# Performance work log

Measured on AMD Instinct MI355X. Metric: run time of the kernel, lower is better.

The kernel has to match this reference:

```python
import jax, jax.numpy as jnp
import numpy as np

N = 50000
E = 400000  # bidirectional: second half is reverse of first half
D = 128
T = 3
EPS = 1e-09


def apply_lambda(x, log_dt, log_lambda_real, lambda_imag, one_minus=False):
    # lambda_complex = exp((-exp(log_lambda_real) + 1j*lambda_imag) * dt)
    dt = jnp.exp(log_dt)
    mag = jnp.exp(-jnp.exp(log_lambda_real) * dt)          # |lambda| [D//2]
    mag = jnp.where(one_minus, 1.0 - mag, mag)
    phase = lambda_imag * dt                                # angle (cos/sin are wrap-invariant)
    c, s = jnp.cos(phase), jnp.sin(phase)
    xp = x.reshape(x.shape[:-1] + (-1, 2))                  # [..., D//2, 2]
    xr = (c * xp[..., 0] - s * xp[..., 1]) * mag
    xi = (s * xp[..., 0] + c * xp[..., 1]) * mag
    return jnp.stack((xr, xi), axis=-1).reshape(x.shape)


def setup_inputs() -> dict:
    key = jax.random.key(0)
    kx, ke1, ke2, k1, k2, k3, k4 = jax.random.split(key, 7)
    x = jax.random.normal(kx, (N, D), dtype=jnp.float32)
    a = jax.random.randint(ke1, (E // 2,), 0, N)
    b = jax.random.randint(ke2, (E // 2,), 0, N)
    edge_index = jnp.stack([jnp.concatenate([a, b]), jnp.concatenate([b, a])], axis=0)
    hidden = D + D
    scale1 = 1.0 / np.sqrt(D)
    scale2 = 1.0 / np.sqrt(hidden)
    return {
        "x": x,
        "edge_index": edge_index,
        "log_dt": jnp.asarray(np.log(0.1), dtype=jnp.float32),
        "log_lambda_real": jnp.full((D // 2,), np.log(0.5), dtype=jnp.float32),
        "lambda_imag": jnp.arange(D // 2, dtype=jnp.float32) * np.pi,
        "W1": jax.random.uniform(k1, (D, hidden), jnp.float32, -scale1, scale1),
        "W2": jax.random.uniform(k2, (D, hidden), jnp.float32, -scale1, scale1),
        "Wp": jax.random.uniform(k3, (hidden, D), jnp.float32, -scale2, scale2),
        "bp": jax.random.uniform(k4, (D,), jnp.float32, -scale2, scale2),
    }


def reference(x, edge_index, log_dt, log_lambda_real, lambda_imag, W1, W2, Wp, bp):
    x_in = x  # dim_in == dim_out -> residual from pre-MLP input
    # MLP: silu(x W1) * (x W2) -> proj
    h = jax.nn.silu(x @ W1) * (x @ W2)
    x = h @ Wp + bp

    lam = lambda v, om=False: apply_lambda(v, log_dt, log_lambda_real, lambda_imag, om)
    src, dst = edge_index[0], edge_index[1]

    deg = jax.ops.segment_sum(jnp.ones((E,), x.dtype), src, num_segments=N)  # [N]
    M = x[src]                                                              # [E, D]
    m = jax.ops.segment_sum(M, dst, num_segments=N)                         # [N, D]

    for _ in range(T):
        M_ji = jnp.concatenate((M[E // 2:], M[:E // 2]), axis=0)            # reverse-edge message
        x_e = x[src]
        deg_e = deg[src][:, None]
        M = jnp.where(deg_e == 1,
                      x_e,
                      lam(x_e, True) + lam(m[src] - M_ji) / (deg_e - 1 + EPS))
        m = jax.ops.segment_sum(M, dst, num_segments=N)

    out = jnp.where(deg[:, None] == 0, x, lam(x, True) + lam(m) / (deg[:, None] + EPS))
    out = jax.nn.relu(out)  # dropout p=0 (eval)
    return x_in + out
```

## Files before the change

### kernel.cpp

```cpp
#include <hip/hip_runtime.h>

#define EPSF 1e-9f

typedef __bf16 bf16x8 __attribute__((ext_vector_type(8)));
typedef float  f32x4  __attribute__((ext_vector_type(4)));
typedef unsigned short ushort_t;
typedef unsigned int uint_t;
typedef ushort_t us8 __attribute__((ext_vector_type(8)));

__device__ __forceinline__ float2 cmul(float cr, float ci, float2 v) {
    return make_float2(cr * v.x - ci * v.y, ci * v.x + cr * v.y);
}

__device__ __forceinline__ ushort_t f2bf(float f) {
    unsigned int u = __float_as_uint(f);
    u += 0x7FFFu + ((u >> 16) & 1u);
    return (ushort_t)(u >> 16);
}

__device__ __forceinline__ float2 bfu2(uint_t u) {
    return make_float2(__uint_as_float(u << 16), __uint_as_float(u & 0xFFFF0000u));
}
__device__ __forceinline__ uint_t packbf(float2 v) {
    return ((uint_t)f2bf(v.y) << 16) | (uint_t)f2bf(v.x);
}

__global__ void k_lamtab(const float* __restrict__ ldt, const float* __restrict__ llr,
                         const float* __restrict__ lim, float* __restrict__ tab) {
    int p = threadIdx.x;
    if (p >= 64) return;
    float dt  = expf(ldt[0]);
    float mag = expf(-expf(llr[p]) * dt);
    float ph  = lim[p] * dt;
    float c = cosf(ph), s = sinf(ph);
    float m2 = mag * mag, m3 = m2 * mag;
    float c2 = c * c - s * s, s2 = 2.f * c * s;
    float c3 = c2 * c - s2 * s, s3 = s2 * c + c2 * s;
    tab[p]        = c * mag;          tab[64 + p]  = s * mag;
    tab[128 + p]  = c * (1.f - mag);  tab[192 + p] = s * (1.f - mag);
    tab[256 + p]  = c2 * m2;          tab[320 + p] = s2 * m2;
    tab[384 + p]  = c3 * m3;          tab[448 + p] = s3 * m3;
}

__global__ void k_prepw(const float* __restrict__ w, ushort_t* __restrict__ wb,
                        int ncols, int nsteps, int total) {
    int tid = blockIdx.x * blockDim.x + threadIdx.x;
    if (tid >= total) return;
    int l  = tid & 63;
    int s  = (tid >> 6) % nsteps;
    int nt = tid / (64 * nsteps);
    int col = nt * 16 + (l & 15);
    int kb  = s * 32 + (l >> 4) * 8;
    us8 d;
#pragma unroll
    for (int j = 0; j < 8; ++j) d[j] = f2bf(w[(size_t)(kb + j) * ncols + col]);
    *(us8*)(wb + (size_t)tid * 8) = d;
}

__global__ void __launch_bounds__(256)
k_mlpf(const float* __restrict__ x, const ushort_t* __restrict__ wb1,
       const ushort_t* __restrict__ wb2, const ushort_t* __restrict__ wpb,
       const float* __restrict__ bp, float* __restrict__ xp,
       ushort_t* __restrict__ xpb, int Mt) {
    __shared__ ushort_t hs[4][2][4096];
    const int wid = threadIdx.x >> 6, l = threadIdx.x & 63;
    const int pair = blockIdx.x * 4 + wid;
    const int mt0 = pair * 2;
    if (mt0 >= Mt) return;
    const bool has1 = (mt0 + 1) < Mt;
    const int llo = l & 15, lhi = l >> 4;

    bf16x8 af[2][4];
#pragma unroll
    for (int m = 0; m < 2; ++m) {
        int mt = (m == 1 && !has1) ? mt0 : (mt0 + m);
        const float* xr = x + (size_t)(mt * 16 + llo) * 128 + lhi * 8;
#pragma unroll
        for (int s = 0; s < 4; ++s) {
            float4 v0 = *(const float4*)(xr + s * 32);
            float4 v1 = *(const float4*)(xr + s * 32 + 4);
            us8 d;
            d[0] = f2bf(v0.x); d[1] = f2bf(v0.y); d[2] = f2bf(v0.z); d[3] = f2bf(v0.w);
            d[4] = f2bf(v1.x); d[5] = f2bf(v1.y); d[6] = f2bf(v1.z); d[7] = f2bf(v1.w);
            af[m][s] = *(bf16x8*)&d;
        }
    }

    const bf16x8* B1 = (const bf16x8*)wb1;
    const bf16x8* B2 = (const bf16x8*)wb2;
    const bf16x8* BP = (const bf16x8*)wpb;
    const f32x4 zero = {0.f, 0.f, 0.f, 0.f};

#pragma unroll 2
    for (int nt = 0; nt < 16; ++nt) {
        bf16x8 b1[4], b2[4];
#pragma unroll
        for (int s = 0; s < 4; ++s) {
            b1[s] = B1[(nt * 4 + s) * 64 + l];
            b2[s] = B2[(nt * 4 + s) * 64 + l];
        }
#pragma unroll
        for (int m = 0; m < 2; ++m) {
            f32x4 a1 = zero, a2 = zero;
#pragma unroll
            for (int s = 0; s < 4; ++s) {
                a1 = __builtin_amdgcn_mfma_f32_16x16x32_bf16(af[m][s], b1[s], a1, 0, 0, 0);
                a2 = __builtin_amdgcn_mfma_f32_16x16x32_bf16(af[m][s], b2[s], a2, 0, 0, 0);
            }
#pragma unroll
            for (int i = 0; i < 4; ++i) {
                float g = a1[i];
                float hv = (g / (1.f + __expf(-g))) * a2[i];
                int r = 4 * lhi + i;
                int byte = (r << 9) + ((nt * 16 + llo) << 1);
                byte ^= (r & 7) << 4;
                hs[wid][m][byte >> 1] = f2bf(hv);
            }
        }
    }

#pragma unroll 2
    for (int nt3 = 0; nt3 < 8; ++nt3) {
        f32x4 acc0 = zero, acc1 = zero;
#pragma unroll
        for (int sg = 0; sg < 8; ++sg) {
            bf16x8 bw = BP[(nt3 * 8 + sg) * 64 + l];
            int byte = (llo << 9) + (sg << 6) + (lhi << 4);
            byte ^= (llo & 7) << 4;
            bf16x8 h0 = *(const bf16x8*)((const char*)hs[wid][0] + byte);
            acc0 = __builtin_amdgcn_mfma_f32_16x16x32_bf16(h0, bw, acc0, 0, 0, 0);
            bf16x8 h1 = *(const bf16x8*)((const char*)hs[wid][1] + byte);
            acc1 = __builtin_amdgcn_mfma_f32_16x16x32_bf16(h1, bw, acc1, 0, 0, 0);
        }
        float bpv = bp[nt3 * 16 + llo];
        {
            const int row0 = mt0 * 16;
#pragma unroll
            for (int i = 0; i < 4; ++i) {
                int r = row0 + 4 * lhi + i;
                float v = acc0[i] + bpv;
                xp[(size_t)r * 128 + nt3 * 16 + llo] = v;
                xpb[(size_t)r * 128 + nt3 * 16 + llo] = f2bf(v);
            }
        }
        if (has1) {
            const int row0 = (mt0 + 1) * 16;
#pragma unroll
            for (int i = 0; i < 4; ++i) {
                int r = row0 + 4 * lhi + i;
                float v = acc1[i] + bpv;
                xp[(size_t)r * 128 + nt3 * 16 + llo] = v;
                xpb[(size_t)r * 128 + nt3 * 16 + llo] = f2bf(v);
            }
        }
    }
}

__global__ void k_hist(const int* __restrict__ ei, int E, int* __restrict__ cnt) {
    int e = blockIdx.x * blockDim.x + threadIdx.x;
    if (e < E) atomicAdd(&cnt[ei[E + e]], 1);
}

__global__ void __launch_bounds__(256)
k_scanA(const int* __restrict__ cnt, int N, int* __restrict__ bsum) {
    __shared__ int s[256];
    int t = threadIdx.x;
    int i = blockIdx.x * 256 + t;
    int v = (i < N) ? cnt[i] : 0;
    s[t] = v;
    __syncthreads();
#pragma unroll
    for (int d = 128; d > 0; d >>= 1) {
        if (t < d) s[t] += s[t + d];
        __syncthreads();
    }
    if (t == 0) bsum[blockIdx.x] = s[0];
}

__global__ void __launch_bounds__(1024)
k_scanB(const int* __restrict__ bsum, int NB, int* __restrict__ bpre,
        int* __restrict__ offN) {
    __shared__ int s[1024];
    int t = threadIdx.x;
    int v = (t < NB) ? bsum[t] : 0;
    s[t] = v;
    __syncthreads();
    for (int d = 1; d < 1024; d <<= 1) {
        int u = (t >= d) ? s[t - d] : 0;
        __syncthreads();
        s[t] += u;
        __syncthreads();
    }
    if (t < NB) bpre[t] = s[t] - v;
    if (t == NB - 1) *offN = s[t];
}

__global__ void __launch_bounds__(256)
k_scanC(const int* __restrict__ cnt, int N, const int* __restrict__ bpre,
        int* __restrict__ off, int* __restrict__ cursor, float* __restrict__ bv) {
    __shared__ int s[256];
    int t = threadIdx.x;
    int i = blockIdx.x * 256 + t;
    int v = (i < N) ? cnt[i] : 0;
    s[t] = v;
    __syncthreads();
    for (int d = 1; d < 256; d <<= 1) {
        int u = (t >= d) ? s[t - d] : 0;
        __syncthreads();
        s[t] += u;
        __syncthreads();
    }
    if (i < N) {
        int excl = bpre[blockIdx.x] + s[t] - v;
        off[i] = excl;
        cursor[i] = excl;
        bv[i] = (v > 1) ? (-1.f / ((float)v - 1.f + EPSF)) : 0.f;
    }
}

__global__ void k_fill(const int* __restrict__ ei, int E,
                       int* __restrict__ cursor, int* __restrict__ csr) {
    int e = blockIdx.x * blockDim.x + threadIdx.x;
    if (e < E) {
        int s = ei[e], d = ei[E + e];
        int p = atomicAdd(&cursor[d], 1);
        csr[p] = s;
    }
}

__global__ void __launch_bounds__(256)
k_passA(const float* __restrict__ xp, const ushort_t* __restrict__ xpb,
        const float* __restrict__ bv, const int* __restrict__ off,
        const int* __restrict__ csr, const float* __restrict__ tab,
        float* __restrict__ Xb, ushort_t* __restrict__ a1b, int N) {
    int tid = blockIdx.x * blockDim.x + threadIdx.x;
    int v = tid >> 6, l = tid & 63;
    if (v >= N) return;
    int beg = off[v], end = off[v + 1];
    float2 m0 = make_float2(0.f, 0.f), xb = make_float2(0.f, 0.f);
    const uint_t* tb = (const uint_t*)xpb;
    int k = beg;
    for (; k + 1 < end; k += 2) {
        int s0 = csr[k], s1 = csr[k + 1];
        uint_t u0 = tb[(size_t)s0 * 64 + l];
        uint_t u1 = tb[(size_t)s1 * 64 + l];
        float b0 = bv[s0], b1 = bv[s1];
        float2 t0 = bfu2(u0), t1v = bfu2(u1);
        m0.x += t0.x + t1v.x;        m0.y += t0.y + t1v.y;
        xb.x += b0 * t0.x + b1 * t1v.x;
        xb.y += b0 * t0.y + b1 * t1v.y;
    }
    if (k < end) {
        int s0 = csr[k];
        float2 t0 = bfu2(tb[(size_t)s0 * 64 + l]);
        float b0 = bv[s0];
        m0.x += t0.x; m0.y += t0.y;
        xb.x += b0 * t0.x; xb.y += b0 * t0.y;
    }
    size_t o = (size_t)v * 128 + 2 * l;
    *(float2*)&Xb[o] = xb;
    float2 xv = *(const float2*)&xp[o];
    int dg = end - beg;
    float L1r = tab[l], L1i = tab[64 + l], O1r = tab[128 + l], O1i = tab[192 + l];
    float Q = 1.f / ((float)dg - 1.f + EPSF);
    float2 t1 = cmul(O1r, O1i, xv);
    float2 t2 = cmul(L1r, L1i, m0);
    float2 a = make_float2(t1.x + Q * t2.x, t1.y + Q * t2.y);
    if (dg == 1) a = xv;
    ((uint_t*)a1b)[(size_t)v * 64 + l] = packbf(a);
}

__global__ void __launch_bounds__(256)
k_passB(const float* __restrict__ xp, const ushort_t* __restrict__ a1b,
        const float* __restrict__ bv, const int* __restrict__ off,
        const int* __restrict__ csr, const float* __restrict__ tab,
        float* __restrict__ Ab1, float* __restrict__ Bv, float* __restrict__ B2v,
        ushort_t* __restrict__ a2b, int N) {
    int tid = blockIdx.x * blockDim.x + threadIdx.x;
    int v = tid >> 6, l = tid & 63;
    if (v >= N) return;
    int beg = off[v], end = off[v + 1];
    float2 A1 = make_float2(0.f, 0.f), ab = make_float2(0.f, 0.f);
    float Bs = 0.f, B2s = 0.f;
    const uint_t* tb = (const uint_t*)a1b;
    int k = beg;
    for (; k + 1 < end; k += 2) {
        int s0 = csr[k], s1 = csr[k + 1];
        uint_t u0 = tb[(size_t)s0 * 64 + l];
        uint_t u1 = tb[(size_t)s1 * 64 + l];
        float b0 = bv[s0], b1 = bv[s1];
        float2 t0 = bfu2(u0), t1v = bfu2(u1);
        A1.x += t0.x + t1v.x;  A1.y += t0.y + t1v.y;
        ab.x += b0 * t0.x + b1 * t1v.x;
        ab.y += b0 * t0.y + b1 * t1v.y;
        Bs += b0 + b1; B2s += b0 * b0 + b1 * b1;
    }
    if (k < end) {
        int s0 = csr[k];
        float2 t0 = bfu2(tb[(size_t)s0 * 64 + l]);
        float b0 = bv[s0];
        A1.x += t0.x; A1.y += t0.y;
        ab.x += b0 * t0.x; ab.y += b0 * t0.y;
        Bs += b0; B2s += b0 * b0;
    }
    size_t o = (size_t)v * 128 + 2 * l;
    *(float2*)&Ab1[o] = ab;
    if (l == 0) { Bv[v] = Bs; B2v[v] = B2s; }
    float2 xv = *(const float2*)&xp[o];
    int dg = end - beg;
    float L1r = tab[l], L1i = tab[64 + l], O1r = tab[128 + l], O1i = tab[192 + l];
    float2 lx = cmul(L1r, L1i, xv);
    float2 m1 = make_float2(A1.x + Bs * lx.x, A1.y + Bs * lx.y);
    float Q = 1.f / ((float)dg - 1.f + EPSF);
    float2 t1 = cmul(O1r, O1i, xv);
    float2 lm = cmul(L1r, L1i, m1);
    float2 a = make_float2(t1.x + Q * lm.x, t1.y + Q * lm.y);
    if (dg == 1) a = xv;
    ((uint_t*)a2b)[(size_t)v * 64 + l] = packbf(a);
}

__global__ void __launch_bounds__(256)
k_passC(const float* __restrict__ xp, const ushort_t* __restrict__ a2b,
        const ushort_t* __restrict__ a1b, const float* __restrict__ Xb,
        const float* __restrict__ bv, const float* __restrict__ Bv,
        const int* __restrict__ off, const int* __restrict__ csr,
        const float* __restrict__ tab, ushort_t* __restrict__ a3b, int N) {
    int tid = blockIdx.x * blockDim.x + threadIdx.x;
    int v = tid >> 6, l = tid & 63;
    if (v >= N) return;
    int beg = off[v], end = off[v + 1];
    float2 A2 = make_float2(0.f, 0.f);
    const uint_t* tb = (const uint_t*)a2b;
    int k = beg;
    for (; k + 1 < end; k += 2) {
        int s0 = csr[k], s1 = csr[k + 1];
        float2 t0 = bfu2(tb[(size_t)s0 * 64 + l]);
        float2 t1v = bfu2(tb[(size_t)s1 * 64 + l]);
        A2.x += t0.x + t1v.x; A2.y += t0.y + t1v.y;
    }
    if (k < end) {
        float2 t0 = bfu2(tb[(size_t)csr[k] * 64 + l]);
        A2.x += t0.x; A2.y += t0.y;
    }
    size_t o = (size_t)v * 128 + 2 * l;
    float2 xv  = *(const float2*)&xp[o];
    float2 a1v = bfu2(((const uint_t*)a1b)[(size_t)v * 64 + l]);
    float2 Xbv = *(const float2*)&Xb[o];
    int dg = end - beg;
    float Bs = Bv[v], bs = bv[v];
    float L1r = tab[l], L1i = tab[64 + l], O1r = tab[128 + l], O1i = tab[192 + l];
    float L2r = tab[256 + l], L2i = tab[320 + l];
    float2 la1 = cmul(L1r, L1i, a1v);
    float2 lxb = cmul(L2r, L2i, Xbv);
    float2 m2 = make_float2(A2.x + Bs * la1.x + bs * lxb.x,
                            A2.y + Bs * la1.y + bs * lxb.y);
    float Q = 1.f / ((float)dg - 1.f + EPSF);
    float2 t1 = cmul(O1r, O1i, xv);
    float2 lm = cmul(L1r, L1i, m2);
    float2 a = make_float2(t1.x + Q * lm.x, t1.y + Q * lm.y);
    if (dg == 1) a = xv;
    ((uint_t*)a3b)[(size_t)v * 64 + l] = packbf(a);
}

__global__ void __launch_bounds__(256)
k_passD(const float* __restrict__ xin, const float* __restrict__ xp,
        const ushort_t* __restrict__ a3b, const ushort_t* __restrict__ a2b,
        const float* __restrict__ Ab1, const float* __restrict__ bv,
        const float* __restrict__ Bv, const float* __restrict__ B2v,
        const int* __restrict__ off, const int* __restrict__ csr,
        const float* __restrict__ tab, float* __restrict__ out, int N) {
    int tid = blockIdx.x * blockDim.x + threadIdx.x;
    int v = tid >> 6, l = tid & 63;
    if (v >= N) return;
    int beg = off[v], end = off[v + 1];
    float2 A3 = make_float2(0.f, 0.f);
    const uint_t* tb = (const uint_t*)a3b;
    int k = beg;
    for (; k + 1 < end; k += 2) {
        int s0 = csr[k], s1 = csr[k + 1];
        float2 t0 = bfu2(tb[(size_t)s0 * 64 + l]);
        float2 t1v = bfu2(tb[(size_t)s1 * 64 + l]);
        A3.x += t0.x + t1v.x; A3.y += t0.y + t1v.y;
    }
    if (k < end) {
        float2 t0 = bfu2(tb[(size_t)csr[k] * 64 + l]);
        A3.x += t0.x; A3.y += t0.y;
    }
    size_t o = (size_t)v * 128 + 2 * l;
    float2 xv  = *(const float2*)&xp[o];
    float2 a2v = bfu2(((const uint_t*)a2b)[(size_t)v * 64 + l]);
    float2 Abv = *(const float2*)&Ab1[o];
    int dg = end - beg;
    float Bs = Bv[v], bs = bv[v], B2s = B2v[v];
    float L1r = tab[l], L1i = tab[64 + l], O1r = tab[128 + l], O1i = tab[192 + l];
    float L2r = tab[256 + l], L2i = tab[320 + l];
    float L3r = tab[384 + l], L3i = tab[448 + l];
    float2 la2 = cmul(L1r, L1i, a2v);
    float2 lab = cmul(L2r, L2i, Abv);
    float2 lx3 = cmul(L3r, L3i, xv);
    float bB2 = bs * B2s;
    float2 m3 = make_float2(A3.x + Bs * la2.x + bs * lab.x + bB2 * lx3.x,
                            A3.y + Bs * la2.y + bs * lab.y + bB2 * lx3.y);
    float2 g;
    if (dg == 0) {
        g = xv;
    } else {
        float inv = 1.f / ((float)dg + EPSF);
        float2 t1 = cmul(O1r, O1i, xv);
        float2 lm = cmul(L1r, L1i, m3);
        g = make_float2(t1.x + lm.x * inv, t1.y + lm.y * inv);
    }
    float2 xi = *(const float2*)&xin[o];
    float2 res = make_float2(xi.x + fmaxf(g.x, 0.f), xi.y + fmaxf(g.y, 0.f));
    *(float2*)&out[o] = res;
}

extern "C" void kernel_launch(void* const* d_in, const int* in_sizes, int n_in,
                              void* d_out, int out_size, void* d_ws, size_t ws_size,
                              hipStream_t stream) {
    const float* x   = (const float*)d_in[0];
    const int*   ei  = (const int*)d_in[1];
    const float* ldt = (const float*)d_in[2];
    const float* llr = (const float*)d_in[3];
    const float* lim = (const float*)d_in[4];
    const float* W1  = (const float*)d_in[5];
    const float* W2  = (const float*)d_in[6];
    const float* Wp  = (const float*)d_in[7];
    const float* bp  = (const float*)d_in[8];
    float* out = (float*)d_out;

    const int N = in_sizes[0] / 128;
    const int E = in_sizes[1] / 2;
    const size_t nd = (size_t)N * 128;
    const int Mt = (N + 15) / 16;
    const int Mt2 = (Mt + 1) / 2;
    const int NB = (N + 255) / 256;

    float* ws  = (float*)d_ws;
    float* xp  = ws;
    float* Xb  = ws + nd;
    float* ab1 = ws + 2 * nd;
    ushort_t* xpb = (ushort_t*)(ws + 3 * nd);
    ushort_t* a1b = xpb + nd;
    ushort_t* a2b = a1b + nd;
    ushort_t* a3b = a2b + nd;

    int*   cnt    = (int*)(a3b + nd);
    int*   off    = cnt + N;
    int*   cursor = off + N + 4;
    float* bv     = (float*)(cursor + N);
    float* Bv     = bv + N;
    float* B2v    = Bv + N;
    float* tab    = B2v + N;
    int*   bsum   = (int*)(tab + 512);
    int*   bpre   = bsum + NB;
    int*   csr    = bpre + NB;
    ushort_t* wb1 = (ushort_t*)(csr + E);
    ushort_t* wb2 = wb1 + 32768;
    ushort_t* wpb = wb2 + 32768;

    const int nodeBlocks = (int)(((size_t)N * 64 + 255) / 256);
    const int eBlocks    = (E + 255) / 256;

    hipMemsetAsync(cnt, 0, (size_t)N * sizeof(int), stream);
    k_lamtab<<<1, 64, 0, stream>>>(ldt, llr, lim, tab);

    k_prepw<<<16, 256, 0, stream>>>(W1, wb1, 256, 4, 16 * 4 * 64);
    k_prepw<<<16, 256, 0, stream>>>(W2, wb2, 256, 4, 16 * 4 * 64);
    k_prepw<<<16, 256, 0, stream>>>(Wp, wpb, 128, 8, 8 * 8 * 64);
    k_mlpf<<<(Mt2 + 3) / 4, 256, 0, stream>>>(x, wb1, wb2, wpb, bp, xp, xpb, Mt);

    k_hist<<<eBlocks, 256, 0, stream>>>(ei, E, cnt);
    k_scanA<<<NB, 256, 0, stream>>>(cnt, N, bsum);
    k_scanB<<<1, 1024, 0, stream>>>(bsum, NB, bpre, &off[N]);
    k_scanC<<<NB, 256, 0, stream>>>(cnt, N, bpre, off, cursor, bv);
    k_fill<<<eBlocks, 256, 0, stream>>>(ei, E, cursor, csr);

    k_passA<<<nodeBlocks, 256, 0, stream>>>(xp, xpb, bv, off, csr, tab, Xb, a1b, N);
    k_passB<<<nodeBlocks, 256, 0, stream>>>(xp, a1b, bv, off, csr, tab, ab1, Bv, B2v, a2b, N);
    k_passC<<<nodeBlocks, 256, 0, stream>>>(xp, a2b, a1b, Xb, bv, Bv, off, csr, tab, a3b, N);
    k_passD<<<nodeBlocks, 256, 0, stream>>>(x, xp, a3b, a2b, ab1, bv, Bv, B2v, off, csr, tab, out, N);
}
```

Baseline: 245.5 us.

## Store node intermediates in bf16 and halve MLP shared memory per wave

The fp32 copies of the projected features and of the Xb and Ab1 intermediates are dropped. All passes now read bf16-packed versions instead, which cuts per-node global traffic in the four aggregation passes and removes the fp32 store in the MLP. The MLP kernel also keeps the second tile's hidden activations packed in registers and reuses one shared buffer, halving LDS use per wave so more waves can be resident. The risks are extra rounding error on the self terms and higher register pressure from the 32-entry register array.

```diff
diff --git a/kernel.cpp b/kernel.cpp
--- a/kernel.cpp
+++ b/kernel.cpp
@@ -60,15 +60,15 @@
 __global__ void __launch_bounds__(256)
 k_mlpf(const float* __restrict__ x, const ushort_t* __restrict__ wb1,
        const ushort_t* __restrict__ wb2, const ushort_t* __restrict__ wpb,
-       const float* __restrict__ bp, float* __restrict__ xp,
-       ushort_t* __restrict__ xpb, int Mt) {
-    __shared__ ushort_t hs[4][2][4096];
+       const float* __restrict__ bp, ushort_t* __restrict__ xpb, int Mt) {
+    __shared__ ushort_t hs[4][4096];
     const int wid = threadIdx.x >> 6, l = threadIdx.x & 63;
     const int pair = blockIdx.x * 4 + wid;
     const int mt0 = pair * 2;
     if (mt0 >= Mt) return;
     const bool has1 = (mt0 + 1) < Mt;
     const int llo = l & 15, lhi = l >> 4;
+    ushort_t* hw = hs[wid];
 
     bf16x8 af[2][4];
 #pragma unroll
@@ -91,7 +91,8 @@
     const bf16x8* BP = (const bf16x8*)wpb;
     const f32x4 zero = {0.f, 0.f, 0.f, 0.f};
 
-#pragma unroll 2
+    uint_t hpk[32];
+#pragma unroll
     for (int nt = 0; nt < 16; ++nt) {
         bf16x8 b1[4], b2[4];
 #pragma unroll
@@ -99,13 +100,12 @@
             b1[s] = B1[(nt * 4 + s) * 64 + l];
             b2[s] = B2[(nt * 4 + s) * 64 + l];
         }
-#pragma unroll
-        for (int m = 0; m < 2; ++m) {
+        {
             f32x4 a1 = zero, a2 = zero;
 #pragma unroll
             for (int s = 0; s < 4; ++s) {
-                a1 = __builtin_amdgcn_mfma_f32_16x16x32_bf16(af[m][s], b1[s], a1, 0, 0, 0);
-                a2 = __builtin_amdgcn_mfma_f32_16x16x32_bf16(af[m][s], b2[s], a2, 0, 0, 0);
+                a1 = __builtin_amdgcn_mfma_f32_16x16x32_bf16(af[0][s], b1[s], a1, 0, 0, 0);
+                a2 = __builtin_amdgcn_mfma_f32_16x16x32_bf16(af[0][s], b2[s], a2, 0, 0, 0);
             }
 #pragma unroll
             for (int i = 0; i < 4; ++i) {
@@ -114,43 +114,78 @@
                 int r = 4 * lhi + i;
                 int byte = (r << 9) + ((nt * 16 + llo) << 1);
                 byte ^= (r & 7) << 4;
-                hs[wid][m][byte >> 1] = f2bf(hv);
+                hw[byte >> 1] = f2bf(hv);
+            }
+        }
+        {
+            f32x4 a1 = zero, a2 = zero;
+#pragma unroll
+            for (int s = 0; s < 4; ++s) {
+                a1 = __builtin_amdgcn_mfma_f32_16x16x32_bf16(af[1][s], b1[s], a1, 0, 0, 0);
+                a2 = __builtin_amdgcn_mfma_f32_16x16x32_bf16(af[1][s], b2[s], a2, 0, 0, 0);
+            }
+#pragma unroll
+            for (int p = 0; p < 2; ++p) {
+                float g0 = a1[2 * p],     h0 = (g0 / (1.f + __expf(-g0))) * a2[2 * p];
+                float g1 = a1[2 * p + 1], h1 = (g1 / (1.f + __expf(-g1))) * a2[2 * p + 1];
+                hpk[nt * 2 + p] = ((uint_t)f2bf(h1) << 16) | (uint_t)f2bf(h0);
             }
         }
     }
 
 #pragma unroll 2
     for (int nt3 = 0; nt3 < 8; ++nt3) {
-        f32x4 acc0 = zero, acc1 = zero;
+        f32x4 acc = zero;
 #pragma unroll
         for (int sg = 0; sg < 8; ++sg) {
             bf16x8 bw = BP[(nt3 * 8 + sg) * 64 + l];
             int byte = (llo << 9) + (sg << 6) + (lhi << 4);
             byte ^= (llo & 7) << 4;
-            bf16x8 h0 = *(const bf16x8*)((const char*)hs[wid][0] + byte);
-            acc0 = __builtin_amdgcn_mfma_f32_16x16x32_bf16(h0, bw, acc0, 0, 0, 0);
-            bf16x8 h1 = *(const bf16x8*)((const char*)hs[wid][1] + byte);
-            acc1 = __builtin_amdgcn_mfma_f32_16x16x32_bf16(h1, bw, acc1, 0, 0, 0);
+            bf16x8 h0 = *(const bf16x8*)((const char*)hw + byte);
+            acc = __builtin_amdgcn_mfma_f32_16x16x32_bf16(h0, bw, acc, 0, 0, 0);
         }
         float bpv = bp[nt3 * 16 + llo];
-        {
-            const int row0 = mt0 * 16;
+        const int row0 = mt0 * 16;
+#pragma unroll
+        for (int i = 0; i < 4; ++i) {
+            int r = row0 + 4 * lhi + i;
+            xpb[(size_t)r * 128 + nt3 * 16 + llo] = f2bf(acc[i] + bpv);
+        }
+    }
+
+    if (has1) {
+#pragma unroll
+        for (int nt = 0; nt < 16; ++nt) {
+#pragma unroll
+            for (int p = 0; p < 2; ++p) {
+                uint_t u = hpk[nt * 2 + p];
+                int r0 = 4 * lhi + 2 * p;
+                int b0 = (r0 << 9) + ((nt * 16 + llo) << 1);
+                b0 ^= (r0 & 7) << 4;
+                hw[b0 >> 1] = (ushort_t)(u & 0xFFFFu);
+                int r1 = r0 + 1;
+                int b1_ = (r1 << 9) + ((nt * 16 + llo) << 1);
+                b1_ ^= (r1 & 7) << 4;
+                hw[b1_ >> 1] = (ushort_t)(u >> 16);
+            }
+        }
+#pragma unroll 2
+        for (int nt3 = 0; nt3 < 8; ++nt3) {
+            f32x4 acc = zero;
+#pragma unroll
+            for (int sg = 0; sg < 8; ++sg) {
+                bf16x8 bw = BP[(nt3 * 8 + sg) * 64 + l];
+                int byte = (llo << 9) + (sg << 6) + (lhi << 4);
+                byte ^= (llo & 7) << 4;
+                bf16x8 h1 = *(const bf16x8*)((const char*)hw + byte);
+                acc = __builtin_amdgcn_mfma_f32_16x16x32_bf16(h1, bw, acc, 0, 0, 0);
+            }
+            float bpv = bp[nt3 * 16 + llo];
+            const int row0 = (mt0 + 1) * 16;
 #pragma unroll
             for (int i = 0; i < 4; ++i) {
                 int r = row0 + 4 * lhi + i;
-                float v = acc0[i] + bpv;
-                xp[(size_t)r * 128 + nt3 * 16 + llo] = v;
-                xpb[(size_t)r * 128 + nt3 * 16 + llo] = f2bf(v);
-            }
-        }
-        if (has1) {
-            const int row0 = (mt0 + 1) * 16;
-#pragma unroll
-            for (int i = 0; i < 4; ++i) {
-                int r = row0 + 4 * lhi + i;
-                float v = acc1[i] + bpv;
-                xp[(size_t)r * 128 + nt3 * 16 + llo] = v;
-                xpb[(size_t)r * 128 + nt3 * 16 + llo] = f2bf(v);
+                xpb[(size_t)r * 128 + nt3 * 16 + llo] = f2bf(acc[i] + bpv);
             }
         }
     }
@@ -229,10 +264,10 @@
 }
 
 __global__ void __launch_bounds__(256)
-k_passA(const float* __restrict__ xp, const ushort_t* __restrict__ xpb,
-        const float* __restrict__ bv, const int* __restrict__ off,
-        const int* __restrict__ csr, const float* __restrict__ tab,
-        float* __restrict__ Xb, ushort_t* __restrict__ a1b, int N) {
+k_passA(const ushort_t* __restrict__ xpb, const float* __restrict__ bv,
+        const int* __restrict__ off, const int* __restrict__ csr,
+        const float* __restrict__ tab, ushort_t* __restrict__ Xbb,
+        ushort_t* __restrict__ a1b, int N) {
     int tid = blockIdx.x * blockDim.x + threadIdx.x;
     int v = tid >> 6, l = tid & 63;
     if (v >= N) return;
@@ -257,9 +292,8 @@
         m0.x += t0.x; m0.y += t0.y;
         xb.x += b0 * t0.x; xb.y += b0 * t0.y;
     }
-    size_t o = (size_t)v * 128 + 2 * l;
-    *(float2*)&Xb[o] = xb;
-    float2 xv = *(const float2*)&xp[o];
+    ((uint_t*)Xbb)[(size_t)v * 64 + l] = packbf(xb);
+    float2 xv = bfu2(tb[(size_t)v * 64 + l]);
     int dg = end - beg;
     float L1r = tab[l], L1i = tab[64 + l], O1r = tab[128 + l], O1i = tab[192 + l];
     float Q = 1.f / ((float)dg - 1.f + EPSF);
@@ -271,10 +305,10 @@
 }
 
 __global__ void __launch_bounds__(256)
-k_passB(const float* __restrict__ xp, const ushort_t* __restrict__ a1b,
+k_passB(const ushort_t* __restrict__ xpb, const ushort_t* __restrict__ a1b,
         const float* __restrict__ bv, const int* __restrict__ off,
         const int* __restrict__ csr, const float* __restrict__ tab,
-        float* __restrict__ Ab1, float* __restrict__ Bv, float* __restrict__ B2v,
+        ushort_t* __restrict__ ab1b, float* __restrict__ Bv, float* __restrict__ B2v,
         ushort_t* __restrict__ a2b, int N) {
     int tid = blockIdx.x * blockDim.x + threadIdx.x;
     int v = tid >> 6, l = tid & 63;
@@ -303,10 +337,9 @@
         ab.x += b0 * t0.x; ab.y += b0 * t0.y;
         Bs += b0; B2s += b0 * b0;
     }
-    size_t o = (size_t)v * 128 + 2 * l;
-    *(float2*)&Ab1[o] = ab;
+    ((uint_t*)ab1b)[(size_t)v * 64 + l] = packbf(ab);
     if (l == 0) { Bv[v] = Bs; B2v[v] = B2s; }
-    float2 xv = *(const float2*)&xp[o];
+    float2 xv = bfu2(((const uint_t*)xpb)[(size_t)v * 64 + l]);
     int dg = end - beg;
     float L1r = tab[l], L1i = tab[64 + l], O1r = tab[128 + l], O1i = tab[192 + l];
     float2 lx = cmul(L1r, L1i, xv);
@@ -320,8 +353,8 @@
 }
 
 __global__ void __launch_bounds__(256)
-k_passC(const float* __restrict__ xp, const ushort_t* __restrict__ a2b,
-        const ushort_t* __restrict__ a1b, const float* __restrict__ Xb,
+k_passC(const ushort_t* __restrict__ xpb, const ushort_t* __restrict__ a2b,
+        const ushort_t* __restrict__ a1b, const ushort_t* __restrict__ Xbb,
         const float* __restrict__ bv, const float* __restrict__ Bv,
         const int* __restrict__ off, const int* __restrict__ csr,
         const float* __restrict__ tab, ushort_t* __restrict__ a3b, int N) {
@@ -342,10 +375,9 @@
         float2 t0 = bfu2(tb[(size_t)csr[k] * 64 + l]);
         A2.x += t0.x; A2.y += t0.y;
     }
-    size_t o = (size_t)v * 128 + 2 * l;
-    float2 xv  = *(const float2*)&xp[o];
+    float2 xv  = bfu2(((const uint_t*)xpb)[(size_t)v * 64 + l]);
     float2 a1v = bfu2(((const uint_t*)a1b)[(size_t)v * 64 + l]);
-    float2 Xbv = *(const float2*)&Xb[o];
+    float2 Xbv = bfu2(((const uint_t*)Xbb)[(size_t)v * 64 + l]);
     int dg = end - beg;
     float Bs = Bv[v], bs = bv[v];
     float L1r = tab[l], L1i = tab[64 + l], O1r = tab[128 + l], O1i = tab[192 + l];
@@ -363,9 +395,9 @@
 }
 
 __global__ void __launch_bounds__(256)
-k_passD(const float* __restrict__ xin, const float* __restrict__ xp,
+k_passD(const float* __restrict__ xin, const ushort_t* __restrict__ xpb,
         const ushort_t* __restrict__ a3b, const ushort_t* __restrict__ a2b,
-        const float* __restrict__ Ab1, const float* __restrict__ bv,
+        const ushort_t* __restrict__ ab1b, const float* __restrict__ bv,
         const float* __restrict__ Bv, const float* __restrict__ B2v,
         const int* __restrict__ off, const int* __restrict__ csr,
         const float* __restrict__ tab, float* __restrict__ out, int N) {
@@ -387,9 +419,9 @@
         A3.x += t0.x; A3.y += t0.y;
     }
     size_t o = (size_t)v * 128 + 2 * l;
-    float2 xv  = *(const float2*)&xp[o];
+    float2 xv  = bfu2(((const uint_t*)xpb)[(size_t)v * 64 + l]);
     float2 a2v = bfu2(((const uint_t*)a2b)[(size_t)v * 64 + l]);
-    float2 Abv = *(const float2*)&Ab1[o];
+    float2 Abv = bfu2(((const uint_t*)ab1b)[(size_t)v * 64 + l]);
     int dg = end - beg;
     float Bs = Bv[v], bs = bv[v], B2s = B2v[v];
     float L1r = tab[l], L1i = tab[64 + l], O1r = tab[128 + l], O1i = tab[192 + l];
@@ -436,16 +468,14 @@
     const int Mt2 = (Mt + 1) / 2;
     const int NB = (N + 255) / 256;
 
-    float* ws  = (float*)d_ws;
-    float* xp  = ws;
-    float* Xb  = ws + nd;
-    float* ab1 = ws + 2 * nd;
-    ushort_t* xpb = (ushort_t*)(ws + 3 * nd);
-    ushort_t* a1b = xpb + nd;
-    ushort_t* a2b = a1b + nd;
-    ushort_t* a3b = a2b + nd;
-
-    int*   cnt    = (int*)(a3b + nd);
+    ushort_t* xpb  = (ushort_t*)d_ws;
+    ushort_t* a1b  = xpb + nd;
+    ushort_t* a2b  = a1b + nd;
+    ushort_t* a3b  = a2b + nd;
+    ushort_t* Xbb  = a3b + nd;
+    ushort_t* ab1b = Xbb + nd;
+
+    int*   cnt    = (int*)(ab1b + nd);
     int*   off    = cnt + N;
     int*   cursor = off + N + 4;
     float* bv     = (float*)(cursor + N);
@@ -468,7 +498,7 @@
     k_prepw<<<16, 256, 0, stream>>>(W1, wb1, 256, 4, 16 * 4 * 64);
     k_prepw<<<16, 256, 0, stream>>>(W2, wb2, 256, 4, 16 * 4 * 64);
     k_prepw<<<16, 256, 0, stream>>>(Wp, wpb, 128, 8, 8 * 8 * 64);
-    k_mlpf<<<(Mt2 + 3) / 4, 256, 0, stream>>>(x, wb1, wb2, wpb, bp, xp, xpb, Mt);
+    k_mlpf<<<(Mt2 + 3) / 4, 256, 0, stream>>>(x, wb1, wb2, wpb, bp, xpb, Mt);
 
     k_hist<<<eBlocks, 256, 0, stream>>>(ei, E, cnt);
     k_scanA<<<NB, 256, 0, stream>>>(cnt, N, bsum);
@@ -476,8 +506,8 @@
     k_scanC<<<NB, 256, 0, stream>>>(cnt, N, bpre, off, cursor, bv);
     k_fill<<<eBlocks, 256, 0, stream>>>(ei, E, cursor, csr);
 
-    k_passA<<<nodeBlocks, 256, 0, stream>>>(xp, xpb, bv, off, csr, tab, Xb, a1b, N);
-    k_passB<<<nodeBlocks, 256, 0, stream>>>(xp, a1b, bv, off, csr, tab, ab1, Bv, B2v, a2b, N);
-    k_passC<<<nodeBlocks, 256, 0, stream>>>(xp, a2b, a1b, Xb, bv, Bv, off, csr, tab, a3b, N);
-    k_passD<<<nodeBlocks, 256, 0, stream>>>(x, xp, a3b, a2b, ab1, bv, Bv, B2v, off, csr, tab, out, N);
-}
+    k_passA<<<nodeBlocks, 256, 0, stream>>>(xpb, bv, off, csr, tab, Xbb, a1b, N);
+    k_passB<<<nodeBlocks, 256, 0, stream>>>(xpb, a1b, bv, off, csr, tab, ab1b, Bv, B2v, a2b, N);
+    k_passC<<<nodeBlocks, 256, 0, stream>>>(xpb, a2b, a1b, Xbb, bv, Bv, off, csr, tab, a3b, N);
+    k_passD<<<nodeBlocks, 256, 0, stream>>>(x, xpb, a3b, a2b, ab1b, bv, Bv, B2v, off, csr, tab, out, N);
+}
```

New measurement: 241.5 us. Within noise of the previous version (-1.6%).
